# Kernel optimization log

Measured on AMD Instinct MI355X. Metric: run time of the kernel, lower is better.

The kernel has to match this reference:

```python
import jax, jax.numpy as jnp
import numpy as np

B, N, D = 4, 1024, 1024
H, DK, DV = 8, 128, 128
EPS = 1e-6


def setup_inputs() -> dict:
    key = jax.random.key(0)
    ks = jax.random.split(key, 16)
    s = 0.02
    return {
        "q_time": jax.random.normal(ks[0], (B, N, D), jnp.float32),
        "k_time": jax.random.normal(ks[1], (B, N, D), jnp.float32),
        "q_feature": jax.random.normal(ks[2], (B, N, D), jnp.float32),
        "k_feature": jax.random.normal(ks[3], (B, N, D), jnp.float32),
        "v": jax.random.normal(ks[4], (B, N, D), jnp.float32),
        "attn_mask": jax.random.randint(ks[5], (B, N, N), 0, 2, jnp.int32),
        "w_qs_time": jax.random.normal(ks[6], (H * DK, D), jnp.float32) * s,
        "w_ks_time": jax.random.normal(ks[7], (H * DK, D), jnp.float32) * s,
        "w_qs_feature": jax.random.normal(ks[8], (H * DV, D), jnp.float32) * s,
        "w_ks_feature": jax.random.normal(ks[9], (H * DV, D), jnp.float32) * s,
        "w_vs": jax.random.normal(ks[10], (H * DV, D), jnp.float32) * s,
        "w_fc": jax.random.normal(ks[11], (D, H * DV), jnp.float32) * s,
        "ln_gamma": jnp.ones((D,), jnp.float32),
        "ln_beta": jnp.zeros((D,), jnp.float32),
    }


def reference(q_time, k_time, q_feature, k_feature, v, attn_mask,
              w_qs_time, w_ks_time, w_qs_feature, w_ks_feature, w_vs,
              w_fc, ln_gamma, ln_beta):
    temp = DK ** 0.5
    residual = v

    def proj(x, w, d):
        # [B,N,D] @ [D, H*d] -> [B,H,N,d]
        return (x @ w.T).reshape(B, N, H, d).transpose(0, 2, 1, 3)

    qt = proj(q_time, w_qs_time, DK)
    kt = proj(k_time, w_ks_time, DK)
    qf = proj(q_feature, w_qs_feature, DV)
    kf = proj(k_feature, w_ks_feature, DV)
    vv = proj(v, w_vs, DV)

    # time attention: [B,H,N,N]
    attn_time = jnp.einsum('bhnd,bhmd->bhnm', qt / temp, kt)
    attn_time = jnp.where(attn_mask[:, None, :, :] == 0, -1e9, attn_time)
    attn_time = jax.nn.softmax(attn_time, axis=-1)

    # feature attention: q_feature^T @ k_feature -> [B,H,DV,DV]
    attn_feature = jnp.einsum('bhnd,bhne->bhde', qf / temp, kf)
    attn_feature = jax.nn.softmax(attn_feature, axis=-1)

    # chained matmuls: (attn_time @ v) @ attn_feature -> [B,H,N,DV]
    out = jnp.einsum('bhnm,bhmd->bhnd', attn_time, vv)
    out = jnp.einsum('bhnd,bhde->bhne', out, attn_feature)

    out = out.transpose(0, 2, 1, 3).reshape(B, N, H * DV)
    out = out @ w_fc.T + residual  # dropout = identity (eval)

    mean = jnp.mean(out, axis=-1, keepdims=True)
    var = jnp.var(out, axis=-1, keepdims=True)
    out = (out - mean) / jnp.sqrt(var + EPS) * ln_gamma + ln_beta
    return out, attn_time, attn_feature
```

## Files before the change

kernel.cpp:

```cpp
#include <hip/hip_runtime.h>
#include <hip/hip_bf16.h>
#include <cstdint>
#include <cstddef>

typedef unsigned short u16;
typedef short v8s __attribute__((ext_vector_type(8)));
typedef float v4f __attribute__((ext_vector_type(4)));
typedef __hip_bfloat16 bf16;

#define PROJ_ELEMS  4194304ull
#define AT_ELEMS    33554432ull
#define INV_TEMP    0.08838834764831845f

__device__ __forceinline__ void store_out(float* p, float v) { *p = v; }
__device__ __forceinline__ void store_out(bf16* p, float v) { *p = __float2bfloat16(v); }

__device__ __forceinline__ v8s load8f(const float* p) {
    const float4 a = *(const float4*)p;
    const float4 b = *(const float4*)(p + 4);
    v8s r;
    bf16 t;
    t = __float2bfloat16(a.x); r[0] = *(const short*)&t;
    t = __float2bfloat16(a.y); r[1] = *(const short*)&t;
    t = __float2bfloat16(a.z); r[2] = *(const short*)&t;
    t = __float2bfloat16(a.w); r[3] = *(const short*)&t;
    t = __float2bfloat16(b.x); r[4] = *(const short*)&t;
    t = __float2bfloat16(b.y); r[5] = *(const short*)&t;
    t = __float2bfloat16(b.z); r[6] = *(const short*)&t;
    t = __float2bfloat16(b.w); r[7] = *(const short*)&t;
    return r;
}

template <typename AT, typename OutT>
__device__ __forceinline__ void gemm_core(
    const AT* __restrict__ Ab, const u16* __restrict__ Bb, OutT* __restrict__ Cb,
    int K, int lda, int ldb, int ldc, float alpha, int m0, int n0)
{
    __shared__ __align__(16) u16 sA[128][32];
    __shared__ __align__(16) u16 sB[128][32];

    const int tid  = threadIdx.x;
    const int lane = tid & 63;
    const int wid  = tid >> 6;
    const int wm = (wid >> 1) * 64;
    const int wn = (wid & 1) * 64;
    const int quad = lane >> 4;
    const int l16  = lane & 15;

    v4f acc[4][4];
    #pragma unroll
    for (int i = 0; i < 4; ++i)
        #pragma unroll
        for (int j = 0; j < 4; ++j)
            acc[i][j] = (v4f){0.f, 0.f, 0.f, 0.f};

    for (int k0 = 0; k0 < K; k0 += 32) {
        #pragma unroll
        for (int it = 0; it < 2; ++it) {
            const int slot = tid + it * 256;
            const int row  = slot >> 2;
            const int cg   = (slot & 3) << 3;
            __builtin_amdgcn_global_load_lds(
                (const __attribute__((address_space(1))) void*)
                    (Bb + (size_t)(n0 + row) * (size_t)ldb + (size_t)(k0 + cg)),
                (__attribute__((address_space(3))) void*)((char*)&sB[0][0] + slot * 16),
                16, 0, 0);
            if constexpr (sizeof(AT) == 2) {
                __builtin_amdgcn_global_load_lds(
                    (const __attribute__((address_space(1))) void*)
                        ((const u16*)Ab + (size_t)(m0 + row) * (size_t)lda + (size_t)(k0 + cg)),
                    (__attribute__((address_space(3))) void*)((char*)&sA[0][0] + slot * 16),
                    16, 0, 0);
            } else {
                *(v8s*)&sA[row][cg] =
                    load8f((const float*)Ab + (size_t)(m0 + row) * (size_t)lda + (size_t)(k0 + cg));
            }
        }
        __syncthreads();

        v8s af[4], bfr[4];
        #pragma unroll
        for (int i = 0; i < 4; ++i) {
            af[i]  = *(const v8s*)&sA[wm + i * 16 + l16][quad * 8];
            bfr[i] = *(const v8s*)&sB[wn + i * 16 + l16][quad * 8];
        }
        #pragma unroll
        for (int i = 0; i < 4; ++i)
            #pragma unroll
            for (int j = 0; j < 4; ++j)
                acc[i][j] = __builtin_amdgcn_mfma_f32_16x16x32_bf16(af[i], bfr[j], acc[i][j], 0, 0, 0);
        __syncthreads();
    }

    #pragma unroll
    for (int i = 0; i < 4; ++i) {
        int rbase = m0 + wm + i * 16 + quad * 4;
        #pragma unroll
        for (int j = 0; j < 4; ++j) {
            int gcol = n0 + wn + j * 16 + l16;
            #pragma unroll
            for (int r = 0; r < 4; ++r)
                store_out(&Cb[(size_t)(rbase + r) * (size_t)ldc + (size_t)gcol],
                          acc[i][j][r] * alpha);
        }
    }
}

template <typename AT, typename OutT>
__global__ __launch_bounds__(256, 2)
void gemm_fast(const AT* __restrict__ A, const u16* __restrict__ B, OutT* __restrict__ C,
               int K, int lda, int ldb, int ldc, int batDiv,
               long long sAo, long long sAi, long long sBo, long long sBi,
               long long sCo, long long sCi, float alpha)
{
    const int z  = blockIdx.z;
    const int zo = z / batDiv;
    const int zi = z - zo * batDiv;
    gemm_core<AT, OutT>(A + (size_t)zo * (size_t)sAo + (size_t)zi * (size_t)sAi,
                        B + (size_t)zo * (size_t)sBo + (size_t)zi * (size_t)sBi,
                        C + (size_t)zo * (size_t)sCo + (size_t)zi * (size_t)sCi,
                        K, lda, ldb, ldc, alpha, blockIdx.y * 128, blockIdx.x * 128);
}

struct P5 { const u16* a[5]; };
__global__ __launch_bounds__(256, 2)
void gemm_proj5(P5 As, const u16* __restrict__ W, u16* __restrict__ C)
{
    const int z = blockIdx.z;
    gemm_core<u16, bf16>(As.a[z], W + (size_t)z * 1048576ull,
                         (bf16*)(C + (size_t)z * PROJ_ELEMS),
                         1024, 1024, 1024, 1024, 1.f, blockIdx.y * 128, blockIdx.x * 128);
}

template <int NT> struct CP { const float* p[NT]; };

template <int NT>
__global__ __launch_bounds__(256)
void cvt_batch(CP<NT> ps, u16* __restrict__ dst, int perElems)
{
    const float* s = ps.p[blockIdx.z];
    u16* d = dst + (size_t)blockIdx.z * (size_t)perElems;
    const int i = (blockIdx.x * 256 + threadIdx.x) * 8;
    *(v8s*)(d + i) = load8f(s + i);
}

struct T3 { const u16* in[3]; u16* out[3]; };
__global__ __launch_bounds__(256)
void transpose3(T3 t3)
{
    __shared__ u16 tile[32][33];
    const int sel = blockIdx.z >> 5;
    const int z   = blockIdx.z & 31;
    const int b = z >> 3, h = z & 7;
    const u16* ib = t3.in[sel] + (size_t)b * 1048576ull + (size_t)h * 128ull;
    u16* ob = t3.out[sel] + (size_t)z * 131072ull;
    const int m0 = blockIdx.x * 32;
    const int d0 = blockIdx.y * 32;
    const int tx = threadIdx.x;
    const int ty = threadIdx.y;
    #pragma unroll
    for (int i = 0; i < 4; ++i)
        tile[ty + i * 8][tx] = ib[(size_t)(m0 + ty + i * 8) * 1024ull + (size_t)(d0 + tx)];
    __syncthreads();
    #pragma unroll
    for (int i = 0; i < 4; ++i)
        ob[(size_t)(d0 + ty + i * 8) * 1024ull + (size_t)(m0 + tx)] = tile[tx][ty + i * 8];
}

__global__ __launch_bounds__(256)
void softmax_time(float* __restrict__ P, const int* __restrict__ mask)
{
    const int r  = blockIdx.x;
    const int bh = r >> 10, n = r & 1023;
    const int b  = bh >> 3;
    float4* prow = (float4*)(P + (size_t)r * 1024ull);
    const int4* mrow = (const int4*)(mask + ((size_t)b * 1024ull + (size_t)n) * 1024ull);
    const int t = threadIdx.x;

    float4 x = prow[t];
    const int4 m = mrow[t];
    x.x = m.x ? x.x : -1e9f;
    x.y = m.y ? x.y : -1e9f;
    x.z = m.z ? x.z : -1e9f;
    x.w = m.w ? x.w : -1e9f;

    float mx = fmaxf(fmaxf(x.x, x.y), fmaxf(x.z, x.w));
    #pragma unroll
    for (int o = 32; o; o >>= 1) mx = fmaxf(mx, __shfl_xor(mx, o));
    __shared__ float redm[4], reds[4];
    const int w = t >> 6;
    if ((t & 63) == 0) redm[w] = mx;
    __syncthreads();
    mx = fmaxf(fmaxf(redm[0], redm[1]), fmaxf(redm[2], redm[3]));

    x.x = __expf(x.x - mx); x.y = __expf(x.y - mx);
    x.z = __expf(x.z - mx); x.w = __expf(x.w - mx);
    float s = x.x + x.y + x.z + x.w;
    #pragma unroll
    for (int o = 32; o; o >>= 1) s += __shfl_xor(s, o);
    if ((t & 63) == 0) reds[w] = s;
    __syncthreads();
    s = reds[0] + reds[1] + reds[2] + reds[3];
    const float inv = 1.f / s;
    x.x *= inv; x.y *= inv; x.z *= inv; x.w *= inv;
    prow[t] = x;
}

__global__ __launch_bounds__(128)
void softmax_feat(const float* __restrict__ F, float* __restrict__ out_af, u16* __restrict__ FT)
{
    const int r = blockIdx.x;
    const int z = r >> 7, d = r & 127;
    const int e = threadIdx.x;
    float x = F[(size_t)r * 128ull + e];
    float mx = x;
    #pragma unroll
    for (int o = 32; o; o >>= 1) mx = fmaxf(mx, __shfl_xor(mx, o));
    __shared__ float redm[2], reds[2];
    const int w = e >> 6;
    if ((e & 63) == 0) redm[w] = mx;
    __syncthreads();
    mx = fmaxf(redm[0], redm[1]);
    float ex = __expf(x - mx);
    float s = ex;
    #pragma unroll
    for (int o = 32; o; o >>= 1) s += __shfl_xor(s, o);
    if ((e & 63) == 0) reds[w] = s;
    __syncthreads();
    s = reds[0] + reds[1];
    float p = ex / s;
    out_af[(size_t)r * 128ull + e] = p;
    bf16 pb = __float2bfloat16(p);
    FT[(size_t)z * 16384ull + (size_t)e * 128ull + d] = *(const u16*)&pb;
}

__global__ __launch_bounds__(256)
void resid_ln(const float* __restrict__ fc, const float* __restrict__ v,
              const float* __restrict__ gamma, const float* __restrict__ beta,
              float* __restrict__ out)
{
    const int r = blockIdx.x;
    const int t = threadIdx.x;
    const float4* fr = (const float4*)(fc + (size_t)r * 1024ull);
    const float4* vr = (const float4*)(v  + (size_t)r * 1024ull);
    float4 a = fr[t], b4 = vr[t];
    float4 x = {a.x + b4.x, a.y + b4.y, a.z + b4.z, a.w + b4.w};
    float s  = x.x + x.y + x.z + x.w;
    float s2 = x.x * x.x + x.y * x.y + x.z * x.z + x.w * x.w;
    #pragma unroll
    for (int o = 32; o; o >>= 1) { s += __shfl_xor(s, o); s2 += __shfl_xor(s2, o); }
    __shared__ float rs[4], rs2[4];
    const int w = t >> 6;
    if ((t & 63) == 0) { rs[w] = s; rs2[w] = s2; }
    __syncthreads();
    s  = rs[0] + rs[1] + rs[2] + rs[3];
    s2 = rs2[0] + rs2[1] + rs2[2] + rs2[3];
    const float mean = s * (1.f / 1024.f);
    const float var  = s2 * (1.f / 1024.f) - mean * mean;
    const float rstd = rsqrtf(var + 1e-6f);
    const float4 g = ((const float4*)gamma)[t];
    const float4 bb = ((const float4*)beta)[t];
    float4 o4 = {(x.x - mean) * rstd * g.x + bb.x,
                 (x.y - mean) * rstd * g.y + bb.y,
                 (x.z - mean) * rstd * g.z + bb.z,
                 (x.w - mean) * rstd * g.w + bb.w};
    ((float4*)(out + (size_t)r * 1024ull))[t] = o4;
}

extern "C" void kernel_launch(void* const* d_in, const int* in_sizes, int n_in,
                              void* d_out, int out_size, void* d_ws, size_t ws_size,
                              hipStream_t stream)
{
    (void)in_sizes; (void)n_in; (void)out_size; (void)ws_size;
    const float* q_time    = (const float*)d_in[0];
    const float* k_time    = (const float*)d_in[1];
    const float* q_feature = (const float*)d_in[2];
    const float* k_feature = (const float*)d_in[3];
    const float* v_in      = (const float*)d_in[4];
    const int*   mask      = (const int*)d_in[5];
    const float* w_qs_t    = (const float*)d_in[6];
    const float* w_ks_t    = (const float*)d_in[7];
    const float* w_qs_f    = (const float*)d_in[8];
    const float* w_ks_f    = (const float*)d_in[9];
    const float* w_vs      = (const float*)d_in[10];
    const float* w_fc      = (const float*)d_in[11];
    const float* gamma     = (const float*)d_in[12];
    const float* beta      = (const float*)d_in[13];

    char* ws = (char*)d_ws;
    const size_t MB = 1ull << 20;
    u16*   act = (u16*)(ws + 0  * MB);
    u16*   wbf = (u16*)(ws + 40 * MB);
    u16*   qt  = (u16*)(ws + 52 * MB);
    u16*   vvT = (u16*)(ws + 0  * MB);
    u16*   qfT = (u16*)(ws + 8  * MB);
    u16*   kfT = (u16*)(ws + 16 * MB);
    u16*   FT  = (u16*)(ws + 24 * MB);
    float* F   = (float*)(ws + 25 * MB);
    u16*   opv = (u16*)(ws + 27 * MB);
    u16*   o2  = (u16*)(ws + 35 * MB);
    float* fc  = (float*)(ws + 52 * MB);
    u16*   kt  = qt + PROJ_ELEMS;
    u16*   qf  = kt + PROJ_ELEMS;
    u16*   kf  = qf + PROJ_ELEMS;
    u16*   vv  = kf + PROJ_ELEMS;
    u16*   wfc = wbf + 5ull * 1048576ull;

    float* out0 = (float*)d_out;
    float* oAT  = out0 + PROJ_ELEMS;
    float* oAF  = out0 + PROJ_ELEMS + AT_ELEMS;

    const dim3 blk(256);

    {
        CP<5> ca; ca.p[0] = q_time; ca.p[1] = k_time; ca.p[2] = q_feature;
                  ca.p[3] = k_feature; ca.p[4] = v_in;
        cvt_batch<5><<<dim3(2048, 1, 5), blk, 0, stream>>>(ca, act, 4194304);
        CP<6> cw; cw.p[0] = w_qs_t; cw.p[1] = w_ks_t; cw.p[2] = w_qs_f;
                  cw.p[3] = w_ks_f; cw.p[4] = w_vs; cw.p[5] = w_fc;
        cvt_batch<6><<<dim3(512, 1, 6), blk, 0, stream>>>(cw, wbf, 1048576);
    }

    {
        P5 ps; for (int i = 0; i < 5; ++i) ps.a[i] = act + (size_t)i * PROJ_ELEMS;
        gemm_proj5<<<dim3(8, 32, 5), blk, 0, stream>>>(ps, wbf, qt);
    }

    {
        T3 t3; t3.in[0] = vv; t3.in[1] = qf; t3.in[2] = kf;
               t3.out[0] = vvT; t3.out[1] = qfT; t3.out[2] = kfT;
        transpose3<<<dim3(32, 4, 96), dim3(32, 8, 1), 0, stream>>>(t3);
    }

    gemm_fast<<<dim3(8, 8, 32), blk, 0, stream>>>(qt, kt, oAT, 128, 1024, 1024, 1024, 8,
        1048576LL, 128LL, 1048576LL, 128LL, 8388608LL, 1048576LL, INV_TEMP);

    softmax_time<<<32768, 256, 0, stream>>>(oAT, mask);

    gemm_fast<<<dim3(1, 1, 32), blk, 0, stream>>>(qfT, kfT, F, 1024, 1024, 1024, 128, 1,
        131072LL, 0LL, 131072LL, 0LL, 16384LL, 0LL, INV_TEMP);

    softmax_feat<<<4096, 128, 0, stream>>>(F, oAF, FT);

    gemm_fast<<<dim3(1, 8, 32), blk, 0, stream>>>((const float*)oAT, vvT, (bf16*)opv, 1024,
        1024, 1024, 128, 1, 1048576LL, 0LL, 131072LL, 0LL, 131072LL, 0LL, 1.f);

    gemm_fast<<<dim3(1, 8, 32), blk, 0, stream>>>(opv, FT, (bf16*)o2, 128,
        128, 128, 1024, 8, 1048576LL, 131072LL, 131072LL, 16384LL, 1048576LL, 128LL, 1.f);

    gemm_fast<<<dim3(8, 32, 1), blk, 0, stream>>>(o2, wfc, fc, 1024, 1024, 1024, 1024, 1,
        0LL, 0LL, 0LL, 0LL, 0LL, 0LL, 1.f);

    resid_ln<<<4096, 256, 0, stream>>>(fc, v_in, gamma, beta, out0);
}
```

Measured before the change: 496.3 us.

## Fuse time-attention QK, masked softmax and PV into one two-pass kernel

Replaces the separate QK^T GEMM, masked softmax and P·V GEMM with one kernel. Its first pass computes row max and sum online. Its second pass recomputes the scores, writes the normalized probabilities once and multiplies them by V from LDS. The int32 mask is packed into bitmasks up front, and the feature-attention GEMM is split over K into partials that the feature softmax sums. This removes several full round trips of the fp32 attention matrix and the int mask through HBM. In exchange it computes QK^T twice, launches only 256 single-occupancy blocks, and writes probabilities with narrow scalar stores.

```diff
diff --git a/kernel.cpp b/kernel.cpp
--- a/kernel.cpp
+++ b/kernel.cpp
@@ -4,6 +4,7 @@
 #include <cstddef>
 
 typedef unsigned short u16;
+typedef unsigned int u32;
 typedef short v8s __attribute__((ext_vector_type(8)));
 typedef float v4f __attribute__((ext_vector_type(4)));
 typedef __hip_bfloat16 bf16;
@@ -11,6 +12,9 @@
 #define PROJ_ELEMS  4194304ull
 #define AT_ELEMS    33554432ull
 #define INV_TEMP    0.08838834764831845f
+
+#define GLOBAL_AS __attribute__((address_space(1)))
+#define LDS_AS    __attribute__((address_space(3)))
 
 __device__ __forceinline__ void store_out(float* p, float v) { *p = v; }
 __device__ __forceinline__ void store_out(bf16* p, float v) { *p = __float2bfloat16(v); }
@@ -61,16 +65,12 @@
             const int row  = slot >> 2;
             const int cg   = (slot & 3) << 3;
             __builtin_amdgcn_global_load_lds(
-                (const __attribute__((address_space(1))) void*)
-                    (Bb + (size_t)(n0 + row) * (size_t)ldb + (size_t)(k0 + cg)),
-                (__attribute__((address_space(3))) void*)((char*)&sB[0][0] + slot * 16),
-                16, 0, 0);
+                (const GLOBAL_AS void*)(Bb + (size_t)(n0 + row) * (size_t)ldb + (size_t)(k0 + cg)),
+                (LDS_AS void*)((char*)&sB[0][0] + slot * 16), 16, 0, 0);
             if constexpr (sizeof(AT) == 2) {
                 __builtin_amdgcn_global_load_lds(
-                    (const __attribute__((address_space(1))) void*)
-                        ((const u16*)Ab + (size_t)(m0 + row) * (size_t)lda + (size_t)(k0 + cg)),
-                    (__attribute__((address_space(3))) void*)((char*)&sA[0][0] + slot * 16),
-                    16, 0, 0);
+                    (const GLOBAL_AS void*)((const u16*)Ab + (size_t)(m0 + row) * (size_t)lda + (size_t)(k0 + cg)),
+                    (LDS_AS void*)((char*)&sA[0][0] + slot * 16), 16, 0, 0);
             } else {
                 *(v8s*)&sA[row][cg] =
                     load8f((const float*)Ab + (size_t)(m0 + row) * (size_t)lda + (size_t)(k0 + cg));
@@ -132,6 +132,16 @@
                          1024, 1024, 1024, 1024, 1.f, blockIdx.y * 128, blockIdx.x * 128);
 }
 
+__global__ __launch_bounds__(256, 2)
+void gemm_feat_sk(const u16* __restrict__ qfT, const u16* __restrict__ kfT, float* __restrict__ Fp)
+{
+    const int kc = blockIdx.x, z = blockIdx.y;
+    gemm_core<u16, float>(qfT + (size_t)z * 131072ull + (size_t)kc * 128ull,
+                          kfT + (size_t)z * 131072ull + (size_t)kc * 128ull,
+                          Fp + ((size_t)kc * 32 + z) * 16384ull,
+                          128, 1024, 1024, 128, INV_TEMP, 0, 0);
+}
+
 template <int NT> struct CP { const float* p[NT]; };
 
 template <int NT>
@@ -142,6 +152,23 @@
     u16* d = dst + (size_t)blockIdx.z * (size_t)perElems;
     const int i = (blockIdx.x * 256 + threadIdx.x) * 8;
     *(v8s*)(d + i) = load8f(s + i);
+}
+
+__global__ __launch_bounds__(256)
+void mask_pack(const int* __restrict__ mask, u32* __restrict__ mb)
+{
+    const int w = blockIdx.x * 256 + threadIdx.x;
+    const int* src = mask + (size_t)w * 32ull;
+    u32 bits = 0;
+    #pragma unroll
+    for (int i = 0; i < 32; i += 4) {
+        int4 v = *(const int4*)(src + i);
+        bits |= (u32)(v.x != 0) << i;
+        bits |= (u32)(v.y != 0) << (i + 1);
+        bits |= (u32)(v.z != 0) << (i + 2);
+        bits |= (u32)(v.w != 0) << (i + 3);
+    }
+    mb[w] = bits;
 }
 
 struct T3 { const u16* in[3]; u16* out[3]; };
@@ -167,52 +194,296 @@
         ob[(size_t)(d0 + ty + i * 8) * 1024ull + (size_t)(m0 + tx)] = tile[tx][ty + i * 8];
 }
 
-__global__ __launch_bounds__(256)
-void softmax_time(float* __restrict__ P, const int* __restrict__ mask)
-{
-    const int r  = blockIdx.x;
-    const int bh = r >> 10, n = r & 1023;
-    const int b  = bh >> 3;
-    float4* prow = (float4*)(P + (size_t)r * 1024ull);
-    const int4* mrow = (const int4*)(mask + ((size_t)b * 1024ull + (size_t)n) * 1024ull);
-    const int t = threadIdx.x;
-
-    float4 x = prow[t];
-    const int4 m = mrow[t];
-    x.x = m.x ? x.x : -1e9f;
-    x.y = m.y ? x.y : -1e9f;
-    x.z = m.z ? x.z : -1e9f;
-    x.w = m.w ? x.w : -1e9f;
-
-    float mx = fmaxf(fmaxf(x.x, x.y), fmaxf(x.z, x.w));
-    #pragma unroll
-    for (int o = 32; o; o >>= 1) mx = fmaxf(mx, __shfl_xor(mx, o));
-    __shared__ float redm[4], reds[4];
-    const int w = t >> 6;
-    if ((t & 63) == 0) redm[w] = mx;
-    __syncthreads();
-    mx = fmaxf(fmaxf(redm[0], redm[1]), fmaxf(redm[2], redm[3]));
-
-    x.x = __expf(x.x - mx); x.y = __expf(x.y - mx);
-    x.z = __expf(x.z - mx); x.w = __expf(x.w - mx);
-    float s = x.x + x.y + x.z + x.w;
-    #pragma unroll
-    for (int o = 32; o; o >>= 1) s += __shfl_xor(s, o);
-    if ((t & 63) == 0) reds[w] = s;
-    __syncthreads();
-    s = reds[0] + reds[1] + reds[2] + reds[3];
-    const float inv = 1.f / s;
-    x.x *= inv; x.y *= inv; x.z *= inv; x.w *= inv;
-    prow[t] = x;
+__global__ __launch_bounds__(256, 1)
+void fused_attn(const u16* __restrict__ qt, const u16* __restrict__ kt,
+                const u16* __restrict__ vvT, const u32* __restrict__ mb,
+                float* __restrict__ oAT, u16* __restrict__ opv)
+{
+    __shared__ __align__(16) u16 sQ[4][128][32];
+    __shared__ __align__(16) u16 sK[128][32];
+    __shared__ __align__(16) u16 sV[128][32];
+    __shared__ __align__(16) u16 sP[4][128][32];
+    __shared__ float Mld[128], Lld[128], redT[128];
+    __shared__ u32 smw[128][4];
+
+    const int z = blockIdx.y;
+    const int b = z >> 3, h = z & 7;
+    const int m0 = blockIdx.x * 128;
+    const u16* qb = qt + (size_t)b * 1048576ull + (size_t)h * 128ull;
+    const u16* kb = kt + (size_t)b * 1048576ull + (size_t)h * 128ull;
+    const u16* vb = vvT + (size_t)z * 131072ull;
+    float* Ob = oAT + (size_t)z * 1048576ull;
+    const u32* mbb = mb + (size_t)b * 32768ull;
+
+    const int tid = threadIdx.x;
+    const int lane = tid & 63, wid = tid >> 6;
+    const int wm = (wid >> 1) * 64, wn = (wid & 1) * 64;
+    const int quad = lane >> 4, l16 = lane & 15;
+    const int wnw = wn >> 5;
+
+    if (tid < 128) { Mld[tid] = -3.0e38f; Lld[tid] = 0.f; }
+
+    #pragma unroll
+    for (int ks = 0; ks < 4; ++ks)
+        #pragma unroll
+        for (int it = 0; it < 2; ++it) {
+            const int slot = tid + it * 256;
+            const int row = slot >> 2, cg = (slot & 3) << 3;
+            __builtin_amdgcn_global_load_lds(
+                (const GLOBAL_AS void*)(qb + (size_t)(m0 + row) * 1024ull + ks * 32 + cg),
+                (LDS_AS void*)((char*)&sQ[ks][0][0] + slot * 16), 16, 0, 0);
+        }
+
+    for (int nt = 0; nt < 8; ++nt) {
+        v4f acc[4][4];
+        #pragma unroll
+        for (int i = 0; i < 4; ++i)
+            #pragma unroll
+            for (int j = 0; j < 4; ++j)
+                acc[i][j] = (v4f){0.f, 0.f, 0.f, 0.f};
+
+        #pragma unroll
+        for (int ks = 0; ks < 4; ++ks) {
+            #pragma unroll
+            for (int it = 0; it < 2; ++it) {
+                const int slot = tid + it * 256;
+                const int row = slot >> 2, cg = (slot & 3) << 3;
+                __builtin_amdgcn_global_load_lds(
+                    (const GLOBAL_AS void*)(kb + (size_t)(nt * 128 + row) * 1024ull + ks * 32 + cg),
+                    (LDS_AS void*)((char*)&sK[0][0] + slot * 16), 16, 0, 0);
+            }
+            __syncthreads();
+            v8s af[4], bfr[4];
+            #pragma unroll
+            for (int i = 0; i < 4; ++i) {
+                af[i]  = *(const v8s*)&sQ[ks][wm + i * 16 + l16][quad * 8];
+                bfr[i] = *(const v8s*)&sK[wn + i * 16 + l16][quad * 8];
+            }
+            #pragma unroll
+            for (int i = 0; i < 4; ++i)
+                #pragma unroll
+                for (int j = 0; j < 4; ++j)
+                    acc[i][j] = __builtin_amdgcn_mfma_f32_16x16x32_bf16(af[i], bfr[j], acc[i][j], 0, 0, 0);
+            __syncthreads();
+        }
+
+        {
+            const int row = tid >> 1, w0 = (tid & 1) * 2;
+            *(uint2*)&smw[row][w0] = *(const uint2*)(mbb + (size_t)(m0 + row) * 32ull + nt * 4 + w0);
+        }
+        __syncthreads();
+
+        float tm[4][4];
+        #pragma unroll
+        for (int i = 0; i < 4; ++i)
+            #pragma unroll
+            for (int r = 0; r < 4; ++r) {
+                tm[i][r] = -3.0e38f;
+                const int rowl = wm + i * 16 + quad * 4 + r;
+                #pragma unroll
+                for (int j = 0; j < 4; ++j) {
+                    const u32 word = smw[rowl][wnw + (j >> 1)];
+                    const int bit = ((j & 1) << 4) + l16;
+                    float s = acc[i][j][r] * INV_TEMP;
+                    s = ((word >> bit) & 1u) ? s : -1e9f;
+                    acc[i][j][r] = s;
+                    tm[i][r] = fmaxf(tm[i][r], s);
+                }
+                #pragma unroll
+                for (int m = 1; m <= 8; m <<= 1)
+                    tm[i][r] = fmaxf(tm[i][r], __shfl_xor(tm[i][r], m));
+            }
+
+        if ((wid & 1) && l16 == 0) {
+            #pragma unroll
+            for (int i = 0; i < 4; ++i)
+                #pragma unroll
+                for (int r = 0; r < 4; ++r)
+                    redT[wm + i * 16 + quad * 4 + r] = tm[i][r];
+        }
+        __syncthreads();
+
+        float scl[4][4];
+        if (!(wid & 1) && l16 == 0) {
+            #pragma unroll
+            for (int i = 0; i < 4; ++i)
+                #pragma unroll
+                for (int r = 0; r < 4; ++r) {
+                    const int rowl = wm + i * 16 + quad * 4 + r;
+                    const float full = fmaxf(tm[i][r], redT[rowl]);
+                    const float oldM = Mld[rowl];
+                    const float newM = fmaxf(oldM, full);
+                    Mld[rowl] = newM;
+                    scl[i][r] = __expf(oldM - newM);
+                }
+        }
+        __syncthreads();
+
+        float ts[4][4];
+        #pragma unroll
+        for (int i = 0; i < 4; ++i)
+            #pragma unroll
+            for (int r = 0; r < 4; ++r) {
+                const int rowl = wm + i * 16 + quad * 4 + r;
+                const float Mv = Mld[rowl];
+                float t = 0.f;
+                #pragma unroll
+                for (int j = 0; j < 4; ++j)
+                    t += __expf(acc[i][j][r] - Mv);
+                #pragma unroll
+                for (int m = 1; m <= 8; m <<= 1)
+                    t += __shfl_xor(t, m);
+                ts[i][r] = t;
+            }
+        if ((wid & 1) && l16 == 0) {
+            #pragma unroll
+            for (int i = 0; i < 4; ++i)
+                #pragma unroll
+                for (int r = 0; r < 4; ++r)
+                    redT[wm + i * 16 + quad * 4 + r] = ts[i][r];
+        }
+        __syncthreads();
+        if (!(wid & 1) && l16 == 0) {
+            #pragma unroll
+            for (int i = 0; i < 4; ++i)
+                #pragma unroll
+                for (int r = 0; r < 4; ++r) {
+                    const int rowl = wm + i * 16 + quad * 4 + r;
+                    Lld[rowl] = Lld[rowl] * scl[i][r] + ts[i][r] + redT[rowl];
+                }
+        }
+        __syncthreads();
+    }
+
+    float Mr[16], IL[16];
+    #pragma unroll
+    for (int i = 0; i < 4; ++i)
+        #pragma unroll
+        for (int r = 0; r < 4; ++r) {
+            const int rowl = wm + i * 16 + quad * 4 + r;
+            Mr[i * 4 + r] = Mld[rowl];
+            IL[i * 4 + r] = 1.f / Lld[rowl];
+        }
+
+    v4f pacc[4][4];
+    #pragma unroll
+    for (int i = 0; i < 4; ++i)
+        #pragma unroll
+        for (int j = 0; j < 4; ++j)
+            pacc[i][j] = (v4f){0.f, 0.f, 0.f, 0.f};
+
+    for (int nt = 0; nt < 8; ++nt) {
+        v4f acc[4][4];
+        #pragma unroll
+        for (int i = 0; i < 4; ++i)
+            #pragma unroll
+            for (int j = 0; j < 4; ++j)
+                acc[i][j] = (v4f){0.f, 0.f, 0.f, 0.f};
+
+        #pragma unroll
+        for (int ks = 0; ks < 4; ++ks) {
+            #pragma unroll
+            for (int it = 0; it < 2; ++it) {
+                const int slot = tid + it * 256;
+                const int row = slot >> 2, cg = (slot & 3) << 3;
+                __builtin_amdgcn_global_load_lds(
+                    (const GLOBAL_AS void*)(kb + (size_t)(nt * 128 + row) * 1024ull + ks * 32 + cg),
+                    (LDS_AS void*)((char*)&sK[0][0] + slot * 16), 16, 0, 0);
+            }
+            __syncthreads();
+            v8s af[4], bfr[4];
+            #pragma unroll
+            for (int i = 0; i < 4; ++i) {
+                af[i]  = *(const v8s*)&sQ[ks][wm + i * 16 + l16][quad * 8];
+                bfr[i] = *(const v8s*)&sK[wn + i * 16 + l16][quad * 8];
+            }
+            #pragma unroll
+            for (int i = 0; i < 4; ++i)
+                #pragma unroll
+                for (int j = 0; j < 4; ++j)
+                    acc[i][j] = __builtin_amdgcn_mfma_f32_16x16x32_bf16(af[i], bfr[j], acc[i][j], 0, 0, 0);
+            __syncthreads();
+        }
+
+        {
+            const int row = tid >> 1, w0 = (tid & 1) * 2;
+            *(uint2*)&smw[row][w0] = *(const uint2*)(mbb + (size_t)(m0 + row) * 32ull + nt * 4 + w0);
+        }
+        __syncthreads();
+
+        #pragma unroll
+        for (int i = 0; i < 4; ++i)
+            #pragma unroll
+            for (int r = 0; r < 4; ++r) {
+                const int rowl = wm + i * 16 + quad * 4 + r;
+                const int idx = i * 4 + r;
+                #pragma unroll
+                for (int j = 0; j < 4; ++j) {
+                    const u32 word = smw[rowl][wnw + (j >> 1)];
+                    const int bit = ((j & 1) << 4) + l16;
+                    float s = acc[i][j][r] * INV_TEMP;
+                    s = ((word >> bit) & 1u) ? s : -1e9f;
+                    const float p = __expf(s - Mr[idx]) * IL[idx];
+                    const int c = wn + j * 16 + l16;
+                    Ob[(size_t)(m0 + rowl) * 1024ull + nt * 128 + c] = p;
+                    bf16 pb = __float2bfloat16(p);
+                    sP[c >> 5][rowl][c & 31] = *(const u16*)&pb;
+                }
+            }
+        __syncthreads();
+
+        #pragma unroll
+        for (int ks = 0; ks < 4; ++ks) {
+            #pragma unroll
+            for (int it = 0; it < 2; ++it) {
+                const int slot = tid + it * 256;
+                const int row = slot >> 2, cg = (slot & 3) << 3;
+                __builtin_amdgcn_global_load_lds(
+                    (const GLOBAL_AS void*)(vb + (size_t)row * 1024ull + nt * 128 + ks * 32 + cg),
+                    (LDS_AS void*)((char*)&sV[0][0] + slot * 16), 16, 0, 0);
+            }
+            __syncthreads();
+            v8s af[4], bfr[4];
+            #pragma unroll
+            for (int i = 0; i < 4; ++i) {
+                af[i]  = *(const v8s*)&sP[ks][wm + i * 16 + l16][quad * 8];
+                bfr[i] = *(const v8s*)&sV[wn + i * 16 + l16][quad * 8];
+            }
+            #pragma unroll
+            for (int i = 0; i < 4; ++i)
+                #pragma unroll
+                for (int j = 0; j < 4; ++j)
+                    pacc[i][j] = __builtin_amdgcn_mfma_f32_16x16x32_bf16(af[i], bfr[j], pacc[i][j], 0, 0, 0);
+            __syncthreads();
+        }
+    }
+
+    u16* opvB = opv + (size_t)z * 131072ull;
+    #pragma unroll
+    for (int i = 0; i < 4; ++i) {
+        const int rbase = m0 + wm + i * 16 + quad * 4;
+        #pragma unroll
+        for (int j = 0; j < 4; ++j) {
+            const int e = wn + j * 16 + l16;
+            #pragma unroll
+            for (int r = 0; r < 4; ++r) {
+                bf16 t = __float2bfloat16(pacc[i][j][r]);
+                opvB[(size_t)(rbase + r) * 128ull + e] = *(const u16*)&t;
+            }
+        }
+    }
 }
 
 __global__ __launch_bounds__(128)
-void softmax_feat(const float* __restrict__ F, float* __restrict__ out_af, u16* __restrict__ FT)
+void softmax_feat(const float* __restrict__ Fp, float* __restrict__ out_af, u16* __restrict__ FT)
 {
     const int r = blockIdx.x;
     const int z = r >> 7, d = r & 127;
     const int e = threadIdx.x;
-    float x = F[(size_t)r * 128ull + e];
+    float x = 0.f;
+    #pragma unroll
+    for (int kc = 0; kc < 8; ++kc)
+        x += Fp[((size_t)kc * 32 + z) * 16384ull + (size_t)d * 128ull + e];
     float mx = x;
     #pragma unroll
     for (int o = 32; o; o >>= 1) mx = fmaxf(mx, __shfl_xor(mx, o));
@@ -296,10 +567,11 @@
     u16*   qfT = (u16*)(ws + 8  * MB);
     u16*   kfT = (u16*)(ws + 16 * MB);
     u16*   FT  = (u16*)(ws + 24 * MB);
-    float* F   = (float*)(ws + 25 * MB);
-    u16*   opv = (u16*)(ws + 27 * MB);
-    u16*   o2  = (u16*)(ws + 35 * MB);
-    float* fc  = (float*)(ws + 52 * MB);
+    float* Fp  = (float*)(ws + 25 * MB);
+    u16*   opv = (u16*)(ws + 41 * MB);
+    u16*   o2  = (u16*)(ws + 52 * MB);
+    float* fc  = (float*)(ws + 60 * MB);
+    u32*   mb  = (u32*)(ws + 92 * MB);
     u16*   kt  = qt + PROJ_ELEMS;
     u16*   qf  = kt + PROJ_ELEMS;
     u16*   kf  = qf + PROJ_ELEMS;
@@ -319,6 +591,7 @@
         CP<6> cw; cw.p[0] = w_qs_t; cw.p[1] = w_ks_t; cw.p[2] = w_qs_f;
                   cw.p[3] = w_ks_f; cw.p[4] = w_vs; cw.p[5] = w_fc;
         cvt_batch<6><<<dim3(512, 1, 6), blk, 0, stream>>>(cw, wbf, 1048576);
+        mask_pack<<<512, blk, 0, stream>>>(mask, mb);
     }
 
     {
@@ -332,18 +605,11 @@
         transpose3<<<dim3(32, 4, 96), dim3(32, 8, 1), 0, stream>>>(t3);
     }
 
-    gemm_fast<<<dim3(8, 8, 32), blk, 0, stream>>>(qt, kt, oAT, 128, 1024, 1024, 1024, 8,
-        1048576LL, 128LL, 1048576LL, 128LL, 8388608LL, 1048576LL, INV_TEMP);
-
-    softmax_time<<<32768, 256, 0, stream>>>(oAT, mask);
-
-    gemm_fast<<<dim3(1, 1, 32), blk, 0, stream>>>(qfT, kfT, F, 1024, 1024, 1024, 128, 1,
-        131072LL, 0LL, 131072LL, 0LL, 16384LL, 0LL, INV_TEMP);
-
-    softmax_feat<<<4096, 128, 0, stream>>>(F, oAF, FT);
-
-    gemm_fast<<<dim3(1, 8, 32), blk, 0, stream>>>((const float*)oAT, vvT, (bf16*)opv, 1024,
-        1024, 1024, 128, 1, 1048576LL, 0LL, 131072LL, 0LL, 131072LL, 0LL, 1.f);
+    gemm_feat_sk<<<dim3(8, 32), blk, 0, stream>>>(qfT, kfT, Fp);
+
+    softmax_feat<<<4096, 128, 0, stream>>>(Fp, oAF, FT);
+
+    fused_attn<<<dim3(8, 32), blk, 0, stream>>>(qt, kt, vvT, mb, oAT, opv);
 
     gemm_fast<<<dim3(1, 8, 32), blk, 0, stream>>>(opv, FT, (bf16*)o2, 128,
         128, 128, 1024, 8, 1048576LL, 131072LL, 131072LL, 16384LL, 1048576LL, 128LL, 1.f);
```

After: 495.4 us. Within noise of the previous version (-0.2%).
